# Optimization experiments

Measured on AMD Instinct MI355X. Metric: run time of the kernel, lower is better.

Reference implementation:

```python
import math
import jax, jax.numpy as jnp
import numpy as np

IN_FEATURES = 2048
OUT_FEATURES = 8192
WINDOW_SIZE = 6
STRIPES = 3
STEP = 1
GTOKEN = 1


def build_sparse_mask(in_f, out_f, window_size=WINDOW_SIZE, stripes=STRIPES, step=STEP, gtoken=GTOKEN):
    # Faithful numpy port of the torch __init__ mask construction (block_size=None).
    pm_r, pm_c = min(in_f, out_f), max(in_f, out_f)
    tmp = np.zeros((pm_r, pm_c), dtype=np.float32)
    stride = int(math.sqrt(pm_r))
    d = pm_c / pm_r
    if math.ceil(d) - d < 0.1:
        d = math.ceil(d)
    elif d - math.floor(d) < 0.1:
        d = math.floor(d)
    for k in range(stripes):
        ps = stride * (2 ** k - 1)
        for i in range(0, pm_r, window_size):
            tmp[ps + i: ps + i + window_size * step, int(i * d): int(i * d + step * d * window_size)] = 1.0
    for k in range(stripes):
        ps = stride * (2 ** k - 1)
        for i in range(0, pm_r, window_size):
            tmp[i: i + window_size * step, int((i + ps) * d): int((ps + i) * d + step * d * window_size)] = 1.0
    tmp[:, :gtoken] = 1.0
    tmp[:gtoken, :] = 1.0
    if in_f <= out_f:
        return tmp.T  # [out_f, in_f]
    return tmp


def setup_inputs() -> dict:
    key = jax.random.key(0)
    kx, kw, kb = jax.random.split(key, 3)
    x = jax.random.normal(kx, (16384, IN_FEATURES), dtype=jnp.float32)
    weight = jax.random.normal(kw, (OUT_FEATURES, IN_FEATURES), dtype=jnp.float32) * 0.02
    bias = jax.random.normal(kb, (OUT_FEATURES,), dtype=jnp.float32) * 0.02
    sparse_mask = jnp.asarray(build_sparse_mask(IN_FEATURES, OUT_FEATURES))  # [out, in]
    return {"x": x, "weight": weight, "bias": bias, "sparse_mask": sparse_mask}


def reference(x, weight, bias, sparse_mask):
    # y = x @ (mask * W)^T + b   ; mask is a static structured-sparse pattern
    return x @ (sparse_mask * weight).T + bias
```

## Files before the change

### kernel.cpp

```cpp
#include <hip/hip_runtime.h>
#include <hip/hip_bf16.h>

#define M_ROWS 16384
#define K_IN   2048
#define N_OUT  8192
#define OG     12
#define NG     683
#define KUMAX  64
#define GPB    4
#define OTW    (OG*GPB)
#define YPAD   52
#define NTO    171
#define MT     256
#define MAXOFF ((K_IN - 1) * (M_ROWS * 2))

__global__ void ninja_xpose(const float* __restrict__ x, __hip_bfloat16* __restrict__ xT) {
    __shared__ float tile[64][65];
    int mt = blockIdx.x, kt = blockIdx.y;
    int t = threadIdx.x;
    int c = t & 63;
    int r4 = t >> 6;
#pragma unroll
    for (int i = 0; i < 16; i++) {
        int r = r4 + i * 4;
        tile[r][c] = x[(size_t)(mt * 64 + r) * K_IN + kt * 64 + c];
    }
    __syncthreads();
#pragma unroll
    for (int i = 0; i < 16; i++) {
        int r = r4 + i * 4;
        xT[(size_t)(kt * 64 + r) * M_ROWS + mt * 64 + c] = __float2bfloat16(tile[c][r]);
    }
}

__global__ void ninja_prep(const float* __restrict__ mask, const float* __restrict__ W,
                           int* __restrict__ koff, int* __restrict__ kuArr,
                           float* __restrict__ Wd) {
    int g = blockIdx.x, t = threadIdx.x;
    int o0 = g * OG;
    int no = min(OG, N_OUT - o0);
    __shared__ int cnt;
    __shared__ int kl[KUMAX];
    if (t == 0) cnt = 0;
    __syncthreads();
    for (int k = t; k < K_IN; k += 256) {
        int any = 0;
        for (int oo = 0; oo < no; oo++) {
            int o = o0 + oo;
            any |= (o != 0) & (mask[(size_t)o * K_IN + k] != 0.0f);
        }
        if (any) {
            int p = atomicAdd(&cnt, 1);
            if (p < KUMAX) kl[p] = k;
        }
    }
    __syncthreads();
    int c = cnt;
    if (c > KUMAX) {
        if (t == 0) kuArr[g] = -1;
        return;
    }
    int kup = (c + 3) & ~3;
    for (int j = c + t; j < kup; j += 256) kl[j] = 0;
    __syncthreads();
    if (t == 0) kuArr[g] = kup;
    for (int j = t; j < KUMAX; j += 256)
        koff[g * KUMAX + j] = (j < kup) ? kl[j] * (M_ROWS * 2) : 0;
    for (int idx = t; idx < KUMAX * OG; idx += 256) {
        int jk = idx / OG, oo = idx - jk * OG;
        float v = 0.0f;
        int o = o0 + oo;
        if (jk < c && oo < no && o != 0) {
            size_t p = (size_t)o * K_IN + kl[jk];
            v = mask[p] * W[p];
        }
        Wd[(size_t)g * (KUMAX * OG) + idx] = v;
    }
}

__global__ __launch_bounds__(256)
void ninja_main(const __hip_bfloat16* __restrict__ xT,
                const float* __restrict__ mask, const float* __restrict__ W,
                const float* __restrict__ bias,
                const int* __restrict__ koff, const int* __restrict__ kuArr,
                const float* __restrict__ Wd, float* __restrict__ y) {
    __shared__ __align__(16) int koffS[GPB][KUMAX];
    __shared__ int   kusS[GPB];
    __shared__ float biasS[OTW];
    __shared__ __align__(16) float ytile[64][YPAD];

    int t = threadIdx.x;
    int og0 = blockIdx.x * GPB;
    int o0  = og0 * OG;

    {
        int g = t >> 6, j = t & 63;
        int gg = og0 + g;
        int v = (gg < NG) ? koff[gg * KUMAX + j] : 0;
        koffS[g][j] = min(max(v, 0), MAXOFF);
    }
    if (t < GPB) kusS[t] = (og0 + t < NG) ? kuArr[og0 + t] : 0;
    if (t < OTW) biasS[t] = (o0 + t < N_OUT) ? bias[o0 + t] : 0.0f;
    __syncthreads();

    int m = blockIdx.y * MT + t;
    const char* xb = reinterpret_cast<const char*>(xT + m);

    float acc[GPB][OG];
#pragma unroll
    for (int g = 0; g < GPB; g++)
#pragma unroll
        for (int oo = 0; oo < OG; oo++) acc[g][oo] = 0.0f;

#pragma unroll
    for (int g = 0; g < GPB; g++) {
        int gg = og0 + g;
        int ku = min(kusS[g], KUMAX);
        const float4* wp = reinterpret_cast<const float4*>(Wd + (size_t)min(gg, NG - 1) * (KUMAX * OG));
        if (ku >= 0) {
            for (int jk = 0; jk < ku; jk += 4) {
                int4 ko = *reinterpret_cast<const int4*>(&koffS[g][jk]);
#pragma unroll
                for (int u = 0; u < 4; u++) {
                    int off = (u == 0) ? ko.x : (u == 1) ? ko.y : (u == 2) ? ko.z : ko.w;
                    float xv = __bfloat162float(
                        *reinterpret_cast<const __hip_bfloat16*>(xb + off));
                    float4 w0 = wp[(jk + u) * 3 + 0];
                    float4 w1 = wp[(jk + u) * 3 + 1];
                    float4 w2 = wp[(jk + u) * 3 + 2];
                    acc[g][0]  = fmaf(xv, w0.x, acc[g][0]);
                    acc[g][1]  = fmaf(xv, w0.y, acc[g][1]);
                    acc[g][2]  = fmaf(xv, w0.z, acc[g][2]);
                    acc[g][3]  = fmaf(xv, w0.w, acc[g][3]);
                    acc[g][4]  = fmaf(xv, w1.x, acc[g][4]);
                    acc[g][5]  = fmaf(xv, w1.y, acc[g][5]);
                    acc[g][6]  = fmaf(xv, w1.z, acc[g][6]);
                    acc[g][7]  = fmaf(xv, w1.w, acc[g][7]);
                    acc[g][8]  = fmaf(xv, w2.x, acc[g][8]);
                    acc[g][9]  = fmaf(xv, w2.y, acc[g][9]);
                    acc[g][10] = fmaf(xv, w2.z, acc[g][10]);
                    acc[g][11] = fmaf(xv, w2.w, acc[g][11]);
                }
            }
        } else {
            int go0 = gg * OG;
            int no = min(OG, N_OUT - go0);
            for (int k = 0; k < K_IN; k++) {
                float xv = __bfloat162float(
                    *reinterpret_cast<const __hip_bfloat16*>(xb + k * (M_ROWS * 2)));
#pragma unroll
                for (int oo = 0; oo < OG; oo++) {
                    float wv = 0.f;
                    if (oo < no) {
                        size_t p = (size_t)(go0 + oo) * K_IN + k;
                        wv = mask[p] * W[p];
                    }
                    acc[g][oo] = fmaf(xv, wv, acc[g][oo]);
                }
            }
        }
    }

    int WID = min(OTW, N_OUT - o0);
    int mbase = blockIdx.y * MT;
#pragma unroll
    for (int cch = 0; cch < 4; cch++) {
        if ((t >> 6) == cch) {
            int r = t & 63;
#pragma unroll
            for (int g = 0; g < GPB; g++)
#pragma unroll
                for (int oo = 0; oo < OG; oo++)
                    ytile[r][g * OG + oo] = acc[g][oo] + biasS[g * OG + oo];
        }
        __syncthreads();
        float4* yb = reinterpret_cast<float4*>(y + (size_t)(mbase + cch * 64) * N_OUT + o0);
        if (WID == 48) {
#pragma unroll
            for (int i = 0; i < 3; i++) {
                int idx = t + i * 256;
                int r = idx / 12, q = idx - r * 12;
                float4 v = *reinterpret_cast<const float4*>(&ytile[r][4 * q]);
                yb[(size_t)r * (N_OUT / 4) + q] = v;
            }
        } else {
#pragma unroll
            for (int i = 0; i < 2; i++) {
                int idx = t + i * 256;
                int r = idx >> 3, q = idx & 7;
                float4 v = *reinterpret_cast<const float4*>(&ytile[r][4 * q]);
                yb[(size_t)r * (N_OUT / 4) + q] = v;
            }
        }
        __syncthreads();
    }
}

__global__ __launch_bounds__(512)
void ninja_gemv0(const __hip_bfloat16* __restrict__ xT,
                 const float* __restrict__ mask, const float* __restrict__ W,
                 const float* __restrict__ bias, float* __restrict__ y) {
    __shared__ float w0[K_IN];
    __shared__ float part[8][64];
    int t = threadIdx.x;
    for (int k = t; k < K_IN; k += 512) w0[k] = mask[k] * W[k];
    __syncthreads();
    int ml = t & 63;
    int kq = t >> 6;
    int m  = blockIdx.x * 64 + ml;
    const __hip_bfloat16* xp = xT + (size_t)(kq * 256) * M_ROWS + m;
    float a = 0.f;
    for (int k = 0; k < 256; k += 8) {
#pragma unroll
        for (int u = 0; u < 8; u++)
            a = fmaf(w0[kq * 256 + k + u],
                     __bfloat162float(xp[(size_t)(k + u) * M_ROWS]), a);
    }
    part[kq][ml] = a;
    __syncthreads();
    if (t < 64) {
        float s = ((part[0][t] + part[1][t]) + (part[2][t] + part[3][t]))
                + ((part[4][t] + part[5][t]) + (part[6][t] + part[7][t]));
        y[(size_t)(blockIdx.x * 64 + t) * N_OUT] = s + bias[0];
    }
}

__global__ void ninja_fallback(const float* __restrict__ x, const float* __restrict__ W,
                               const float* __restrict__ bias, const float* __restrict__ mask,
                               float* __restrict__ y) {
    int ot = blockIdx.x, mtile = blockIdx.y, t = threadIdx.x;
    int mloc = t & 63;
    int q = t >> 6;
    int m = mtile * 64 + mloc;
    int obase = ot * 64 + q * 16;
    float acc[16];
#pragma unroll
    for (int i = 0; i < 16; i++) acc[i] = 0.0f;
    __shared__ float xs[32][65];
    for (int kt = 0; kt < K_IN; kt += 32) {
#pragma unroll
        for (int j = 0; j < 8; j++) {
            int idx = t + j * 256;
            int r = idx >> 5, cc = idx & 31;
            xs[cc][r] = x[(size_t)(mtile * 64 + r) * K_IN + kt + cc];
        }
        __syncthreads();
        for (int kk = 0; kk < 32; kk++) {
            float xv = xs[kk][mloc];
#pragma unroll
            for (int i = 0; i < 16; i++) {
                size_t p = (size_t)(obase + i) * K_IN + kt + kk;
                acc[i] = fmaf(xv, mask[p] * W[p], acc[i]);
            }
        }
        __syncthreads();
    }
#pragma unroll
    for (int i = 0; i < 16; i++) acc[i] += bias[obase + i];
    float4* yp = reinterpret_cast<float4*>(y + (size_t)m * N_OUT + obase);
#pragma unroll
    for (int i = 0; i < 4; i++)
        yp[i] = make_float4(acc[4 * i], acc[4 * i + 1], acc[4 * i + 2], acc[4 * i + 3]);
}

extern "C" void kernel_launch(void* const* d_in, const int* in_sizes, int n_in,
                              void* d_out, int out_size, void* d_ws, size_t ws_size,
                              hipStream_t stream) {
    const float* x    = (const float*)d_in[0];
    const float* W    = (const float*)d_in[1];
    const float* bias = (const float*)d_in[2];
    const float* mask = (const float*)d_in[3];
    float* y = (float*)d_out;

    size_t xT_bytes    = (size_t)K_IN * M_ROWS * sizeof(__hip_bfloat16);
    size_t koff_off    = xT_bytes;
    size_t koff_bytes  = (size_t)NG * KUMAX * sizeof(int);
    size_t ku_off      = koff_off + ((koff_bytes + 255) & ~(size_t)255);
    size_t ku_bytes    = ((size_t)NG * sizeof(int) + 255) & ~(size_t)255;
    size_t wd_off      = ku_off + ku_bytes;
    size_t wd_bytes    = (size_t)NG * KUMAX * OG * sizeof(float);
    size_t needed      = wd_off + wd_bytes;

    if (ws_size < needed) {
        ninja_fallback<<<dim3(N_OUT / 64, M_ROWS / 64), 256, 0, stream>>>(x, W, bias, mask, y);
        return;
    }

    char* ws = (char*)d_ws;
    __hip_bfloat16* xT = (__hip_bfloat16*)ws;
    int*   koff  = (int*)(ws + koff_off);
    int*   kuArr = (int*)(ws + ku_off);
    float* Wd    = (float*)(ws + wd_off);

    ninja_xpose<<<dim3(M_ROWS / 64, K_IN / 64), 256, 0, stream>>>(x, xT);
    ninja_prep<<<dim3(NG), 256, 0, stream>>>(mask, W, koff, kuArr, Wd);
    ninja_main<<<dim3(NTO, M_ROWS / MT), 256, 0, stream>>>(xT, mask, W, bias, koff, kuArr, Wd, y);
    ninja_gemv0<<<dim3(M_ROWS / 64), 512, 0, stream>>>(xT, mask, W, bias, y);
}
```

Measured before the change: 887.9 us.

## Compute two rows per thread with packed bf16 loads; vectorize transpose

The main kernel now has each thread handle two adjacent M rows. It loads a 32-bit pair of bf16 values and keeps two accumulator sets, so each weight float4 load and each gathered offset serves twice as much work. MT doubles to 512 and the output epilogue is reorganized into 8 chunks of 32 threads. The transpose kernel now uses float4 reads and packed ushort4 bf16 writes. The extra accumulators double register pressure (96 floats), which may lower occupancy or cause spills.

```diff
diff --git a/kernel.cpp b/kernel.cpp
--- a/kernel.cpp
+++ b/kernel.cpp
@@ -11,25 +11,43 @@
 #define OTW    (OG*GPB)
 #define YPAD   52
 #define NTO    171
-#define MT     256
+#define MT     512
 #define MAXOFF ((K_IN - 1) * (M_ROWS * 2))
 
-__global__ void ninja_xpose(const float* __restrict__ x, __hip_bfloat16* __restrict__ xT) {
-    __shared__ float tile[64][65];
+__global__ __launch_bounds__(256)
+void ninja_xpose(const float* __restrict__ x, __hip_bfloat16* __restrict__ xT) {
+    __shared__ float tile[64][66];
     int mt = blockIdx.x, kt = blockIdx.y;
     int t = threadIdx.x;
-    int c = t & 63;
-    int r4 = t >> 6;
-#pragma unroll
-    for (int i = 0; i < 16; i++) {
-        int r = r4 + i * 4;
-        tile[r][c] = x[(size_t)(mt * 64 + r) * K_IN + kt * 64 + c];
-    }
-    __syncthreads();
-#pragma unroll
-    for (int i = 0; i < 16; i++) {
-        int r = r4 + i * 4;
-        xT[(size_t)(kt * 64 + r) * M_ROWS + mt * 64 + c] = __float2bfloat16(tile[c][r]);
+    int r  = t >> 4;
+    int c4 = (t & 15) * 4;
+#pragma unroll
+    for (int p = 0; p < 4; p++) {
+        int ro = r + p * 16;
+        float4 v = *reinterpret_cast<const float4*>(
+            &x[(size_t)(mt * 64 + ro) * K_IN + kt * 64 + c4]);
+        tile[c4 + 0][ro] = v.x;
+        tile[c4 + 1][ro] = v.y;
+        tile[c4 + 2][ro] = v.z;
+        tile[c4 + 3][ro] = v.w;
+    }
+    __syncthreads();
+    int kloc = t >> 4;
+    int m4   = (t & 15) * 4;
+#pragma unroll
+    for (int p = 0; p < 4; p++) {
+        int ko = kloc + p * 16;
+        float f0 = tile[ko][m4 + 0];
+        float f1 = tile[ko][m4 + 1];
+        float f2 = tile[ko][m4 + 2];
+        float f3 = tile[ko][m4 + 3];
+        ushort4 u;
+        u.x = __hip_bfloat16_raw(__float2bfloat16(f0)).x;
+        u.y = __hip_bfloat16_raw(__float2bfloat16(f1)).x;
+        u.z = __hip_bfloat16_raw(__float2bfloat16(f2)).x;
+        u.w = __hip_bfloat16_raw(__float2bfloat16(f3)).x;
+        *reinterpret_cast<ushort4*>(
+            &xT[(size_t)(kt * 64 + ko) * M_ROWS + mt * 64 + m4]) = u;
     }
 }
 
@@ -103,51 +121,54 @@
     if (t < OTW) biasS[t] = (o0 + t < N_OUT) ? bias[o0 + t] : 0.0f;
     __syncthreads();
 
-    int m = blockIdx.y * MT + t;
-    const char* xb = reinterpret_cast<const char*>(xT + m);
-
-    float acc[GPB][OG];
+    int m0 = blockIdx.y * MT + 2 * t;
+    const char* xb = reinterpret_cast<const char*>(xT) + 2 * (size_t)m0;
+
+    float accA[GPB][OG], accB[GPB][OG];
 #pragma unroll
     for (int g = 0; g < GPB; g++)
 #pragma unroll
-        for (int oo = 0; oo < OG; oo++) acc[g][oo] = 0.0f;
+        for (int oo = 0; oo < OG; oo++) { accA[g][oo] = 0.0f; accB[g][oo] = 0.0f; }
 
 #pragma unroll
     for (int g = 0; g < GPB; g++) {
         int gg = og0 + g;
         int ku = min(kusS[g], KUMAX);
-        const float4* wp = reinterpret_cast<const float4*>(Wd + (size_t)min(gg, NG - 1) * (KUMAX * OG));
+        const float4* wp = reinterpret_cast<const float4*>(
+            Wd + (size_t)min(gg, NG - 1) * (KUMAX * OG));
         if (ku >= 0) {
             for (int jk = 0; jk < ku; jk += 4) {
                 int4 ko = *reinterpret_cast<const int4*>(&koffS[g][jk]);
 #pragma unroll
                 for (int u = 0; u < 4; u++) {
                     int off = (u == 0) ? ko.x : (u == 1) ? ko.y : (u == 2) ? ko.z : ko.w;
-                    float xv = __bfloat162float(
-                        *reinterpret_cast<const __hip_bfloat16*>(xb + off));
+                    unsigned int xv = *reinterpret_cast<const unsigned int*>(xb + off);
+                    float xa = __uint_as_float(xv << 16);
+                    float xc = __uint_as_float(xv & 0xffff0000u);
                     float4 w0 = wp[(jk + u) * 3 + 0];
                     float4 w1 = wp[(jk + u) * 3 + 1];
                     float4 w2 = wp[(jk + u) * 3 + 2];
-                    acc[g][0]  = fmaf(xv, w0.x, acc[g][0]);
-                    acc[g][1]  = fmaf(xv, w0.y, acc[g][1]);
-                    acc[g][2]  = fmaf(xv, w0.z, acc[g][2]);
-                    acc[g][3]  = fmaf(xv, w0.w, acc[g][3]);
-                    acc[g][4]  = fmaf(xv, w1.x, acc[g][4]);
-                    acc[g][5]  = fmaf(xv, w1.y, acc[g][5]);
-                    acc[g][6]  = fmaf(xv, w1.z, acc[g][6]);
-                    acc[g][7]  = fmaf(xv, w1.w, acc[g][7]);
-                    acc[g][8]  = fmaf(xv, w2.x, acc[g][8]);
-                    acc[g][9]  = fmaf(xv, w2.y, acc[g][9]);
-                    acc[g][10] = fmaf(xv, w2.z, acc[g][10]);
-                    acc[g][11] = fmaf(xv, w2.w, acc[g][11]);
+                    accA[g][0]  = fmaf(xa, w0.x, accA[g][0]);  accB[g][0]  = fmaf(xc, w0.x, accB[g][0]);
+                    accA[g][1]  = fmaf(xa, w0.y, accA[g][1]);  accB[g][1]  = fmaf(xc, w0.y, accB[g][1]);
+                    accA[g][2]  = fmaf(xa, w0.z, accA[g][2]);  accB[g][2]  = fmaf(xc, w0.z, accB[g][2]);
+                    accA[g][3]  = fmaf(xa, w0.w, accA[g][3]);  accB[g][3]  = fmaf(xc, w0.w, accB[g][3]);
+                    accA[g][4]  = fmaf(xa, w1.x, accA[g][4]);  accB[g][4]  = fmaf(xc, w1.x, accB[g][4]);
+                    accA[g][5]  = fmaf(xa, w1.y, accA[g][5]);  accB[g][5]  = fmaf(xc, w1.y, accB[g][5]);
+                    accA[g][6]  = fmaf(xa, w1.z, accA[g][6]);  accB[g][6]  = fmaf(xc, w1.z, accB[g][6]);
+                    accA[g][7]  = fmaf(xa, w1.w, accA[g][7]);  accB[g][7]  = fmaf(xc, w1.w, accB[g][7]);
+                    accA[g][8]  = fmaf(xa, w2.x, accA[g][8]);  accB[g][8]  = fmaf(xc, w2.x, accB[g][8]);
+                    accA[g][9]  = fmaf(xa, w2.y, accA[g][9]);  accB[g][9]  = fmaf(xc, w2.y, accB[g][9]);
+                    accA[g][10] = fmaf(xa, w2.z, accA[g][10]); accB[g][10] = fmaf(xc, w2.z, accB[g][10]);
+                    accA[g][11] = fmaf(xa, w2.w, accA[g][11]); accB[g][11] = fmaf(xc, w2.w, accB[g][11]);
                 }
             }
         } else {
             int go0 = gg * OG;
             int no = min(OG, N_OUT - go0);
             for (int k = 0; k < K_IN; k++) {
-                float xv = __bfloat162float(
-                    *reinterpret_cast<const __hip_bfloat16*>(xb + k * (M_ROWS * 2)));
+                unsigned int xv = *reinterpret_cast<const unsigned int*>(xb + k * (M_ROWS * 2));
+                float xa = __uint_as_float(xv << 16);
+                float xc = __uint_as_float(xv & 0xffff0000u);
 #pragma unroll
                 for (int oo = 0; oo < OG; oo++) {
                     float wv = 0.f;
@@ -155,7 +176,8 @@
                         size_t p = (size_t)(go0 + oo) * K_IN + k;
                         wv = mask[p] * W[p];
                     }
-                    acc[g][oo] = fmaf(xv, wv, acc[g][oo]);
+                    accA[g][oo] = fmaf(xa, wv, accA[g][oo]);
+                    accB[g][oo] = fmaf(xc, wv, accB[g][oo]);
                 }
             }
         }
@@ -164,14 +186,17 @@
     int WID = min(OTW, N_OUT - o0);
     int mbase = blockIdx.y * MT;
 #pragma unroll
-    for (int cch = 0; cch < 4; cch++) {
-        if ((t >> 6) == cch) {
-            int r = t & 63;
+    for (int cch = 0; cch < 8; cch++) {
+        if ((t >> 5) == cch) {
+            int r = (t & 31) * 2;
 #pragma unroll
             for (int g = 0; g < GPB; g++)
 #pragma unroll
-                for (int oo = 0; oo < OG; oo++)
-                    ytile[r][g * OG + oo] = acc[g][oo] + biasS[g * OG + oo];
+                for (int oo = 0; oo < OG; oo++) {
+                    float b = biasS[g * OG + oo];
+                    ytile[r][g * OG + oo]     = accA[g][oo] + b;
+                    ytile[r + 1][g * OG + oo] = accB[g][oo] + b;
+                }
         }
         __syncthreads();
         float4* yb = reinterpret_cast<float4*>(y + (size_t)(mbase + cch * 64) * N_OUT + o0);
```

Result: no change. 880.2 us (-0.9%).
